# Kernel tuning notes

Measured on AMD Instinct MI355X. Metric: run time of the kernel, lower is better.

The kernel has to match this reference:

```python
import jax, jax.numpy as jnp
import numpy as np
from jax.ops import segment_sum

N = 100000
E = 1600000
D_IN = 64
D_H = 64
D_OUT = 16


def _gcn_norm(edge_index, n_nodes):
    # PyG GCNConv default: add self-loops, symmetric normalization.
    src, dst = edge_index[0], edge_index[1]
    loop = jnp.arange(n_nodes, dtype=edge_index.dtype)
    src = jnp.concatenate([src, loop])
    dst = jnp.concatenate([dst, loop])
    deg = segment_sum(jnp.ones(src.shape[0], dtype=jnp.float32), dst, num_segments=n_nodes)
    dinv = jnp.where(deg > 0, jax.lax.rsqrt(deg), 0.0)
    norm = dinv[src] * dinv[dst]  # [E + N]
    return src, dst, norm


def _gcn_layer(x, W, b, src, dst, norm, n_nodes):
    h = x @ W  # dense transform first (out_channels <= in_channels)
    msg = h[src] * norm[:, None]          # gather + scale  [E+N, out]
    agg = segment_sum(msg, dst, num_segments=n_nodes)  # scatter-add
    return agg + b


def setup_inputs() -> dict:
    key = jax.random.key(0)
    ks = jax.random.split(key, 10)
    x = jax.random.normal(ks[0], (N, D_IN), dtype=jnp.float32)
    edge_index = jax.random.randint(ks[1], (2, E), 0, N, dtype=jnp.int64)

    def glorot(k, fan_in, fan_out):
        lim = np.sqrt(6.0 / (fan_in + fan_out)).astype(np.float32)
        return jax.random.uniform(k, (fan_in, fan_out), jnp.float32, -lim, lim)

    return {
        "x": x,
        "edge_index": edge_index,
        "W1": glorot(ks[2], D_IN, D_H), "b1": jnp.zeros((D_H,), jnp.float32),
        "W2": glorot(ks[3], D_H, D_H), "b2": jnp.zeros((D_H,), jnp.float32),
        "W3": glorot(ks[4], D_H, D_H), "b3": jnp.zeros((D_H,), jnp.float32),
        "W4": glorot(ks[5], D_H, D_OUT), "b4": jnp.zeros((D_OUT,), jnp.float32),
    }


def reference(x, edge_index, W1, b1, W2, b2, W3, b3, W4, b4):
    n = x.shape[0]
    src, dst, norm = _gcn_norm(edge_index, n)
    h = jax.nn.relu(_gcn_layer(x, W1, b1, src, dst, norm, n))
    h = jax.nn.relu(_gcn_layer(h, W2, b2, src, dst, norm, n))
    h = jax.nn.relu(_gcn_layer(h, W3, b3, src, dst, norm, n))
    return _gcn_layer(h, W4, b4, src, dst, norm, n)
```

## Files before the change

kernel.cpp:

```cpp
#include <hip/hip_runtime.h>
#include <hip/hip_fp16.h>

#define NN 100000
#define NE 1600000
#define BK 256
#define BKSH 8
#define NBKT 391
#define SLOT 4608
#define SRCMASK 0x1FFFF

typedef _Float16 half2v __attribute__((ext_vector_type(2)));

__device__ inline float dot2acc(unsigned int a, unsigned int b, float c) {
#if __has_builtin(__builtin_amdgcn_fdot2)
    union { unsigned int u; half2v h; } ua, ub;
    ua.u = a; ub.u = b;
    return __builtin_amdgcn_fdot2(ua.h, ub.h, c, false);
#else
    float2 fa = __half22float2(*(const __half2*)&a);
    float2 fb = __half22float2(*(const __half2*)&b);
    return c + fa.x * fb.x + fa.y * fb.y;
#endif
}

__device__ inline int wave_incl_scan(int v, int lane) {
#pragma unroll
    for (int off = 1; off < 64; off <<= 1) {
        int t = __shfl_up(v, off, 64);
        if (lane >= off) v += t;
    }
    return v;
}


__global__ __launch_bounds__(512) void bscatter_kernel(const int* __restrict__ src,
                                                       const int* __restrict__ dst,
                                                       int* __restrict__ cnt,
                                                       int* __restrict__ bcur,
                                                       unsigned int* __restrict__ bedges,
                                                       int e) {
    __shared__ int h[512];
    __shared__ int gb[512];
    int tid = threadIdx.x;
    int tile = blockIdx.x * 4096;
    int cnt_tile = min(4096, e - tile);
    h[tid] = 0;
    __syncthreads();
    unsigned int pk[8]; int rk[8], bk[8];
#pragma unroll
    for (int j = 0; j < 8; j++) {
        int li = tid + j * 512;
        if (li < cnt_tile) {
            int s = src[tile + li];
            int d = dst[tile + li];
            bk[j] = d >> BKSH;
            pk[j] = ((unsigned)(d & (BK - 1)) << 17) | (unsigned)s;
            rk[j] = atomicAdd(&h[bk[j]], 1);
            atomicAdd(&cnt[d], 1);
        } else bk[j] = -1;
    }
    __syncthreads();
    {
        int c = h[tid];
        if (c > 0) gb[tid] = atomicAdd(&bcur[tid], c);
    }
    __syncthreads();
#pragma unroll
    for (int j = 0; j < 8; j++)
        if (bk[j] >= 0)
            bedges[(size_t)bk[j] * SLOT + gb[bk[j]] + rk[j]] = pk[j];
}

__global__ __launch_bounds__(512) void bfill_kernel(const unsigned int* __restrict__ bedges,
                                                    const int* __restrict__ bcur,
                                                    const int* __restrict__ cnt,
                                                    const float* __restrict__ x,
                                                    int* __restrict__ start,
                                                    float* __restrict__ dinv,
                                                    int* __restrict__ csr,
                                                    __half* __restrict__ g) {
    __shared__ int lcnt[BK];
    __shared__ int lstart[BK];
    __shared__ int lcur[BK];
    int q = blockIdx.x, tid = threadIdx.x;
    size_t ebase = (size_t)q * SLOT;
    int ec = bcur[q];
    int nbase = q * BK;
    if (tid < BK) {
        int nd = nbase + tid;
        lcnt[tid] = (nd < NN) ? cnt[nd] : 0;
    }
    unsigned int pk[9];
#pragma unroll
    for (int k = 0; k < 9; k++) {
        int i = tid + k * 512;
        pk[k] = (i < ec) ? __builtin_nontemporal_load(&bedges[ebase + i]) : 0xFFFFFFFFu;
    }
    __syncthreads();
    if (tid < 64) {
        int b0 = tid * 4;
        int c0 = lcnt[b0], c1 = lcnt[b0 + 1], c2 = lcnt[b0 + 2], c3 = lcnt[b0 + 3];
        int s4 = c0 + c1 + c2 + c3;
        int incl = wave_incl_scan(s4, tid);
        int base = incl - s4;
        lstart[b0] = base;               lcur[b0] = base;
        lstart[b0 + 1] = base + c0;      lcur[b0 + 1] = base + c0;
        lstart[b0 + 2] = base + c0 + c1; lcur[b0 + 2] = base + c0 + c1;
        lstart[b0 + 3] = base + c0 + c1 + c2; lcur[b0 + 3] = base + c0 + c1 + c2;
    }
    __syncthreads();
    if (tid < BK) {
        int nd = nbase + tid;
        if (nd < NN) {
            start[nd] = (int)ebase + lstart[tid];
            dinv[nd]  = rsqrtf((float)lcnt[tid] + 1.0f);
        }
    }
#pragma unroll
    for (int k = 0; k < 9; k++) {
        if (pk[k] != 0xFFFFFFFFu) {
            int r = atomicAdd(&lcur[pk[k] >> 17], 1);
            csr[ebase + r] = (int)(pk[k] & SRCMASK);
        }
    }
    int nh = NN - nbase; if (nh > BK) nh = BK;
    for (int i = tid; i < nh * 16; i += 512) {
        int r = i >> 4, c4 = (i & 15) << 2;
        float dvv = rsqrtf((float)lcnt[r] + 1.0f);
        size_t off = (size_t)(nbase + r) * 64 + c4;
        float4 v = *(const float4*)&x[off];
        union { __half2 h[2]; uint2 u; } pq;
        pq.h[0] = __floats2half2_rn(v.x * dvv, v.y * dvv);
        pq.h[1] = __floats2half2_rn(v.z * dvv, v.w * dvv);
        *(uint2*)&g[off] = pq.u;
    }
}

__global__ __launch_bounds__(512) void fused_layer_kernel(const __half* __restrict__ g,
                                                          const int* __restrict__ csr,
                                                          const int* __restrict__ start,
                                                          const int* __restrict__ cnt,
                                                          const float* __restrict__ dinv,
                                                          const float* __restrict__ Wg,
                                                          const float* __restrict__ bias,
                                                          __half* __restrict__ gout, int n) {
    __shared__ uint4 wpk[8][64];
    __shared__ __half zh[8][64];
    __shared__ float bs[64];
    int tid = threadIdx.x;
    {
        int p = tid >> 6, c = tid & 63;
        float w[8];
#pragma unroll
        for (int i = 0; i < 8; i++) w[i] = Wg[(8 * p + i) * 64 + c];
        union { __half2 h; unsigned int u; } u0, u1, u2, u3;
        u0.h = __floats2half2_rn(w[0], w[1]);
        u1.h = __floats2half2_rn(w[2], w[3]);
        u2.h = __floats2half2_rn(w[4], w[5]);
        u3.h = __floats2half2_rn(w[6], w[7]);
        wpk[p][c] = make_uint4(u0.u, u1.u, u2.u, u3.u);
    }
    if (tid < 64) bs[tid] = bias[tid];
    __syncthreads();

    int wv = tid >> 6, lane = tid & 63;
    int node = blockIdx.x * 8 + wv;
    float acc = 0.f;
    float dv = 0.f;
    if (node < n) {
        int st = __builtin_amdgcn_readfirstlane(start[node]);
        int cn = __builtin_amdgcn_readfirstlane(cnt[node]);
        dv = dinv[node];
        acc = __half2float(g[(size_t)node * 64 + lane]);
        int e = 0;
        for (; e + 7 < cn; e += 8) {
            int u[8]; float a[8];
#pragma unroll
            for (int j = 0; j < 8; j++) u[j] = __builtin_nontemporal_load(&csr[st + e + j]);
#pragma unroll
            for (int j = 0; j < 8; j++) a[j] = __half2float(g[(size_t)u[j] * 64 + lane]);
            acc += ((a[0] + a[1]) + (a[2] + a[3])) + ((a[4] + a[5]) + (a[6] + a[7]));
        }
        for (; e + 3 < cn; e += 4) {
            int u0 = __builtin_nontemporal_load(&csr[st + e + 0]);
            int u1 = __builtin_nontemporal_load(&csr[st + e + 1]);
            int u2 = __builtin_nontemporal_load(&csr[st + e + 2]);
            int u3 = __builtin_nontemporal_load(&csr[st + e + 3]);
            float a0 = __half2float(g[(size_t)u0 * 64 + lane]);
            float a1 = __half2float(g[(size_t)u1 * 64 + lane]);
            float a2 = __half2float(g[(size_t)u2 * 64 + lane]);
            float a3 = __half2float(g[(size_t)u3 * 64 + lane]);
            acc += (a0 + a1) + (a2 + a3);
        }
        for (; e < cn; e++) {
            int u = __builtin_nontemporal_load(&csr[st + e]);
            acc += __half2float(g[(size_t)u * 64 + lane]);
        }
    }
    zh[wv][lane] = __float2half_rn(acc);
    if (node < n) {
        float t = 0.f;
#pragma unroll
        for (int p = 0; p < 8; p++) {
            uint4 wq = wpk[p][lane];
            uint4 zq = *(const uint4*)&zh[wv][p * 8];
            t = dot2acc(zq.x, wq.x, t);
            t = dot2acc(zq.y, wq.y, t);
            t = dot2acc(zq.z, wq.z, t);
            t = dot2acc(zq.w, wq.w, t);
        }
        float o = dv * t + bs[lane];
        o = fmaxf(o, 0.f);
        gout[(size_t)node * 64 + lane] = __float2half_rn(dv * o);
    }
}

__global__ __launch_bounds__(512) void fused_last_kernel(const __half* __restrict__ g,
                                                         const int* __restrict__ csr,
                                                         const int* __restrict__ start,
                                                         const int* __restrict__ cnt,
                                                         const float* __restrict__ dinv,
                                                         const float* __restrict__ Wg,
                                                         const float* __restrict__ bias,
                                                         const float* __restrict__ W4,
                                                         __half* __restrict__ s4out, int n) {
    __shared__ uint4 wpk[8][64];
    __shared__ __half zh[8][64];
    __shared__ __half z2[8][64];
    __shared__ uint4 w4pk[8][16];
    __shared__ float bs[64];
    int tid = threadIdx.x;
    {
        int p = tid >> 6, c = tid & 63;
        float w[8];
#pragma unroll
        for (int i = 0; i < 8; i++) w[i] = Wg[(8 * p + i) * 64 + c];
        union { __half2 h; unsigned int u; } u0, u1, u2, u3;
        u0.h = __floats2half2_rn(w[0], w[1]);
        u1.h = __floats2half2_rn(w[2], w[3]);
        u2.h = __floats2half2_rn(w[4], w[5]);
        u3.h = __floats2half2_rn(w[6], w[7]);
        wpk[p][c] = make_uint4(u0.u, u1.u, u2.u, u3.u);
    }
    if (tid < 128) {
        int p = tid >> 4, j = tid & 15;
        float w[8];
#pragma unroll
        for (int i = 0; i < 8; i++) w[i] = W4[(8 * p + i) * 16 + j];
        union { __half2 h; unsigned int u; } u0, u1, u2, u3;
        u0.h = __floats2half2_rn(w[0], w[1]);
        u1.h = __floats2half2_rn(w[2], w[3]);
        u2.h = __floats2half2_rn(w[4], w[5]);
        u3.h = __floats2half2_rn(w[6], w[7]);
        w4pk[p][j] = make_uint4(u0.u, u1.u, u2.u, u3.u);
    }
    if (tid < 64) bs[tid] = bias[tid];
    __syncthreads();

    int wv = tid >> 6, lane = tid & 63;
    int node = blockIdx.x * 8 + wv;
    float acc = 0.f;
    float dv = 0.f;
    if (node < n) {
        int st = __builtin_amdgcn_readfirstlane(start[node]);
        int cn = __builtin_amdgcn_readfirstlane(cnt[node]);
        dv = dinv[node];
        acc = __half2float(g[(size_t)node * 64 + lane]);
        int e = 0;
        for (; e + 7 < cn; e += 8) {
            int u[8]; float a[8];
#pragma unroll
            for (int j = 0; j < 8; j++) u[j] = __builtin_nontemporal_load(&csr[st + e + j]);
#pragma unroll
            for (int j = 0; j < 8; j++) a[j] = __half2float(g[(size_t)u[j] * 64 + lane]);
            acc += ((a[0] + a[1]) + (a[2] + a[3])) + ((a[4] + a[5]) + (a[6] + a[7]));
        }
        for (; e + 3 < cn; e += 4) {
            int u0 = __builtin_nontemporal_load(&csr[st + e + 0]);
            int u1 = __builtin_nontemporal_load(&csr[st + e + 1]);
            int u2 = __builtin_nontemporal_load(&csr[st + e + 2]);
            int u3 = __builtin_nontemporal_load(&csr[st + e + 3]);
            float a0 = __half2float(g[(size_t)u0 * 64 + lane]);
            float a1 = __half2float(g[(size_t)u1 * 64 + lane]);
            float a2 = __half2float(g[(size_t)u2 * 64 + lane]);
            float a3 = __half2float(g[(size_t)u3 * 64 + lane]);
            acc += (a0 + a1) + (a2 + a3);
        }
        for (; e < cn; e++) {
            int u = __builtin_nontemporal_load(&csr[st + e]);
            acc += __half2float(g[(size_t)u * 64 + lane]);
        }
    }
    zh[wv][lane] = __float2half_rn(acc);
    if (node < n) {
        float t = 0.f;
#pragma unroll
        for (int p = 0; p < 8; p++) {
            uint4 wq = wpk[p][lane];
            uint4 zq = *(const uint4*)&zh[wv][p * 8];
            t = dot2acc(zq.x, wq.x, t);
            t = dot2acc(zq.y, wq.y, t);
            t = dot2acc(zq.z, wq.z, t);
            t = dot2acc(zq.w, wq.w, t);
        }
        float o = dv * t + bs[lane];
        o = fmaxf(o, 0.f);
        z2[wv][lane] = __float2half_rn(dv * o);
        int col = lane & 15, seg = lane >> 4;
        float t4 = 0.f;
#pragma unroll
        for (int pp = 0; pp < 2; pp++) {
            int p = seg * 2 + pp;
            uint4 wq = w4pk[p][col];
            uint4 zq = *(const uint4*)&z2[wv][p * 8];
            t4 = dot2acc(zq.x, wq.x, t4);
            t4 = dot2acc(zq.y, wq.y, t4);
            t4 = dot2acc(zq.z, wq.z, t4);
            t4 = dot2acc(zq.w, wq.w, t4);
        }
        t4 += __shfl_xor(t4, 16, 64);
        t4 += __shfl_xor(t4, 32, 64);
        if (lane < 16)
            s4out[(size_t)node * 16 + col] = __float2half_rn(t4);
    }
}

__global__ __launch_bounds__(256) void agg16_kernel(const __half* __restrict__ s,
                                                    const int* __restrict__ csr,
                                                    const int* __restrict__ start,
                                                    const int* __restrict__ cnt,
                                                    const float* __restrict__ dinv,
                                                    const float* __restrict__ bias,
                                                    float* __restrict__ out, int n) {
    constexpr int D = 16;
    int tid = threadIdx.x;
    int lane = tid & 63;
    int wave = tid >> 6;
    int col = lane % D;
    int grp = lane / D;
    int node = (blockIdx.x * 4 + wave) * 4 + grp;
    if (node >= n) return;
    int st = start[node];
    int cn = cnt[node];
    float acc = __half2float(s[(size_t)node * D + col]);
    int e = 0;
    for (; e + 7 < cn; e += 8) {
        int u[8]; float a[8];
#pragma unroll
        for (int j = 0; j < 8; j++) u[j] = __builtin_nontemporal_load(&csr[st + e + j]);
#pragma unroll
        for (int j = 0; j < 8; j++) a[j] = __half2float(s[(size_t)u[j] * D + col]);
        acc += ((a[0] + a[1]) + (a[2] + a[3])) + ((a[4] + a[5]) + (a[6] + a[7]));
    }
    for (; e + 3 < cn; e += 4) {
        int u0 = __builtin_nontemporal_load(&csr[st + e + 0]);
        int u1 = __builtin_nontemporal_load(&csr[st + e + 1]);
        int u2 = __builtin_nontemporal_load(&csr[st + e + 2]);
        int u3 = __builtin_nontemporal_load(&csr[st + e + 3]);
        float a0 = __half2float(s[(size_t)u0 * D + col]);
        float a1 = __half2float(s[(size_t)u1 * D + col]);
        float a2 = __half2float(s[(size_t)u2 * D + col]);
        float a3 = __half2float(s[(size_t)u3 * D + col]);
        acc += (a0 + a1) + (a2 + a3);
    }
    for (; e < cn; e++) {
        int u = __builtin_nontemporal_load(&csr[st + e]);
        acc += __half2float(s[(size_t)u * D + col]);
    }
    float o = dinv[node] * acc + bias[col];
    __builtin_nontemporal_store(o, out + (size_t)node * D + col);
}


extern "C" void kernel_launch(void* const* d_in, const int* in_sizes, int n_in,
                              void* d_out, int out_size, void* d_ws, size_t ws_size,
                              hipStream_t stream) {
    const float* x  = (const float*)d_in[0];
    const int* ei   = (const int*)d_in[1];
    const float* W1 = (const float*)d_in[2];
    const float* b1 = (const float*)d_in[3];
    const float* W2 = (const float*)d_in[4];
    const float* b2 = (const float*)d_in[5];
    const float* W3 = (const float*)d_in[6];
    const float* b3 = (const float*)d_in[7];
    const float* W4 = (const float*)d_in[8];
    const float* b4 = (const float*)d_in[9];
    const int* src = ei;
    const int* dst = ei + NE;

    char* w = (char*)d_ws;
    float* dinv  = (float*)w;          w += (size_t)NN * 4;
    int* cnt     = (int*)w;            w += (size_t)NN * 4;
    int* bcur    = (int*)w;            w += (size_t)512 * 4;
    int* start   = (int*)w;            w += (size_t)NN * 4;
    int* csr     = (int*)w;            w += (size_t)NBKT * SLOT * 4;
    __half* gA   = (__half*)w;         w += (size_t)NN * 64 * 2;
    __half* gB   = (__half*)w;         w += (size_t)NN * 64 * 2;
    __half* s4   = (__half*)w;         w += (size_t)NN * 16 * 2;
    unsigned int* bedges = (unsigned int*)w;  w += (size_t)NBKT * SLOT * 4;

    hipMemsetAsync(cnt, 0, (size_t)NN * 4 + 512 * 4, stream);
    bscatter_kernel<<<(NE + 4095) / 4096, 512, 0, stream>>>(src, dst, cnt, bcur, bedges, NE);
    bfill_kernel<<<NBKT, 512, 0, stream>>>(bedges, bcur, cnt, x, start, dinv, csr, gA);

    const int FB = (NN + 7) / 8;
    fused_layer_kernel<<<FB, 512, 0, stream>>>(gA, csr, start, cnt, dinv, W1, b1, gB, NN);
    fused_layer_kernel<<<FB, 512, 0, stream>>>(gB, csr, start, cnt, dinv, W2, b2, gA, NN);
    fused_last_kernel<<<FB, 512, 0, stream>>>(gA, csr, start, cnt, dinv, W3, b3, W4, s4, NN);

    const int AB16 = (NN + 15) / 16;
    agg16_kernel<<<AB16, 256, 0, stream>>>(s4, csr, start, cnt, dinv, b4, (float*)d_out, NN);
}
```

Baseline: 364.7 us.

## Count degrees in shared memory and gather two neighbors per wave with half2 loads

Degree counting moves out of the global-atomic scatter pass and into the per-bucket fill kernel, where it uses shared-memory atomics over the bucket's edges. That removes 1.6M global atomics and shrinks the memset to just the bucket cursors. The aggregation loops in the fused layer kernels now split each wave into two 32-lane halves, each loading half2 pairs from a different neighbor, then combine with a cross-half shuffle. This issues fewer, wider gather loads per edge, at the cost of a shuffle reduction and more register pressure from the 16-edge unroll.

```diff
diff --git a/kernel.cpp b/kernel.cpp
--- a/kernel.cpp
+++ b/kernel.cpp
@@ -35,7 +35,6 @@
 
 __global__ __launch_bounds__(512) void bscatter_kernel(const int* __restrict__ src,
                                                        const int* __restrict__ dst,
-                                                       int* __restrict__ cnt,
                                                        int* __restrict__ bcur,
                                                        unsigned int* __restrict__ bedges,
                                                        int e) {
@@ -56,7 +55,6 @@
             bk[j] = d >> BKSH;
             pk[j] = ((unsigned)(d & (BK - 1)) << 17) | (unsigned)s;
             rk[j] = atomicAdd(&h[bk[j]], 1);
-            atomicAdd(&cnt[d], 1);
         } else bk[j] = -1;
     }
     __syncthreads();
@@ -73,9 +71,9 @@
 
 __global__ __launch_bounds__(512) void bfill_kernel(const unsigned int* __restrict__ bedges,
                                                     const int* __restrict__ bcur,
-                                                    const int* __restrict__ cnt,
                                                     const float* __restrict__ x,
                                                     int* __restrict__ start,
+                                                    int* __restrict__ cnt,
                                                     float* __restrict__ dinv,
                                                     int* __restrict__ csr,
                                                     __half* __restrict__ g) {
@@ -86,16 +84,17 @@
     size_t ebase = (size_t)q * SLOT;
     int ec = bcur[q];
     int nbase = q * BK;
-    if (tid < BK) {
-        int nd = nbase + tid;
-        lcnt[tid] = (nd < NN) ? cnt[nd] : 0;
-    }
+    if (tid < BK) lcnt[tid] = 0;
+    __syncthreads();
     unsigned int pk[9];
 #pragma unroll
     for (int k = 0; k < 9; k++) {
         int i = tid + k * 512;
         pk[k] = (i < ec) ? __builtin_nontemporal_load(&bedges[ebase + i]) : 0xFFFFFFFFu;
     }
+#pragma unroll
+    for (int k = 0; k < 9; k++)
+        if (pk[k] != 0xFFFFFFFFu) atomicAdd(&lcnt[pk[k] >> 17], 1);
     __syncthreads();
     if (tid < 64) {
         int b0 = tid * 4;
@@ -113,6 +112,7 @@
         int nd = nbase + tid;
         if (nd < NN) {
             start[nd] = (int)ebase + lstart[tid];
+            cnt[nd]   = lcnt[tid];
             dinv[nd]  = rsqrtf((float)lcnt[tid] + 1.0f);
         }
     }
@@ -164,40 +164,66 @@
     __syncthreads();
 
     int wv = tid >> 6, lane = tid & 63;
+    int hv = lane >> 5;
+    int c2 = lane & 31;
     int node = blockIdx.x * 8 + wv;
-    float acc = 0.f;
-    float dv = 0.f;
+    float ax = 0.f, ay = 0.f, dv = 0.f;
     if (node < n) {
         int st = __builtin_amdgcn_readfirstlane(start[node]);
         int cn = __builtin_amdgcn_readfirstlane(cnt[node]);
         dv = dinv[node];
-        acc = __half2float(g[(size_t)node * 64 + lane]);
+        {
+            unsigned int sv = *(const unsigned int*)(g + (size_t)node * 64 + 2 * c2);
+            float2 sf = __half22float2(*(const __half2*)&sv);
+            if (hv == 0) { ax = sf.x; ay = sf.y; }
+        }
         int e = 0;
+        for (; e + 15 < cn; e += 16) {
+            int u[16];
+#pragma unroll
+            for (int j = 0; j < 16; j++) u[j] = __builtin_nontemporal_load(&csr[st + e + j]);
+            float2 f[8];
+#pragma unroll
+            for (int j = 0; j < 8; j++) {
+                int us = hv ? u[2 * j + 1] : u[2 * j];
+                unsigned int v = *(const unsigned int*)(g + (size_t)us * 64 + 2 * c2);
+                f[j] = __half22float2(*(const __half2*)&v);
+            }
+            ax += ((f[0].x + f[1].x) + (f[2].x + f[3].x)) + ((f[4].x + f[5].x) + (f[6].x + f[7].x));
+            ay += ((f[0].y + f[1].y) + (f[2].y + f[3].y)) + ((f[4].y + f[5].y) + (f[6].y + f[7].y));
+        }
         for (; e + 7 < cn; e += 8) {
-            int u[8]; float a[8];
+            int u[8];
 #pragma unroll
             for (int j = 0; j < 8; j++) u[j] = __builtin_nontemporal_load(&csr[st + e + j]);
-#pragma unroll
-            for (int j = 0; j < 8; j++) a[j] = __half2float(g[(size_t)u[j] * 64 + lane]);
-            acc += ((a[0] + a[1]) + (a[2] + a[3])) + ((a[4] + a[5]) + (a[6] + a[7]));
-        }
-        for (; e + 3 < cn; e += 4) {
-            int u0 = __builtin_nontemporal_load(&csr[st + e + 0]);
+            float2 f[4];
+#pragma unroll
+            for (int j = 0; j < 4; j++) {
+                int us = hv ? u[2 * j + 1] : u[2 * j];
+                unsigned int v = *(const unsigned int*)(g + (size_t)us * 64 + 2 * c2);
+                f[j] = __half22float2(*(const __half2*)&v);
+            }
+            ax += (f[0].x + f[1].x) + (f[2].x + f[3].x);
+            ay += (f[0].y + f[1].y) + (f[2].y + f[3].y);
+        }
+        for (; e + 1 < cn; e += 2) {
+            int u0 = __builtin_nontemporal_load(&csr[st + e]);
             int u1 = __builtin_nontemporal_load(&csr[st + e + 1]);
-            int u2 = __builtin_nontemporal_load(&csr[st + e + 2]);
-            int u3 = __builtin_nontemporal_load(&csr[st + e + 3]);
-            float a0 = __half2float(g[(size_t)u0 * 64 + lane]);
-            float a1 = __half2float(g[(size_t)u1 * 64 + lane]);
-            float a2 = __half2float(g[(size_t)u2 * 64 + lane]);
-            float a3 = __half2float(g[(size_t)u3 * 64 + lane]);
-            acc += (a0 + a1) + (a2 + a3);
-        }
-        for (; e < cn; e++) {
-            int u = __builtin_nontemporal_load(&csr[st + e]);
-            acc += __half2float(g[(size_t)u * 64 + lane]);
-        }
-    }
-    zh[wv][lane] = __float2half_rn(acc);
+            int us = hv ? u1 : u0;
+            unsigned int v = *(const unsigned int*)(g + (size_t)us * 64 + 2 * c2);
+            float2 f = __half22float2(*(const __half2*)&v);
+            ax += f.x; ay += f.y;
+        }
+        if (e < cn) {
+            int u0 = __builtin_nontemporal_load(&csr[st + e]);
+            unsigned int v = *(const unsigned int*)(g + (size_t)u0 * 64 + 2 * c2);
+            float2 f = __half22float2(*(const __half2*)&v);
+            if (hv == 0) { ax += f.x; ay += f.y; }
+        }
+        ax += __shfl_xor(ax, 32, 64);
+        ay += __shfl_xor(ay, 32, 64);
+    }
+    *(__half2*)&zh[wv][2 * c2] = __floats2half2_rn(ax, ay);
     if (node < n) {
         float t = 0.f;
 #pragma unroll
@@ -258,40 +284,66 @@
     __syncthreads();
 
     int wv = tid >> 6, lane = tid & 63;
+    int hv = lane >> 5;
+    int c2 = lane & 31;
     int node = blockIdx.x * 8 + wv;
-    float acc = 0.f;
-    float dv = 0.f;
+    float ax = 0.f, ay = 0.f, dv = 0.f;
     if (node < n) {
         int st = __builtin_amdgcn_readfirstlane(start[node]);
         int cn = __builtin_amdgcn_readfirstlane(cnt[node]);
         dv = dinv[node];
-        acc = __half2float(g[(size_t)node * 64 + lane]);
+        {
+            unsigned int sv = *(const unsigned int*)(g + (size_t)node * 64 + 2 * c2);
+            float2 sf = __half22float2(*(const __half2*)&sv);
+            if (hv == 0) { ax = sf.x; ay = sf.y; }
+        }
         int e = 0;
+        for (; e + 15 < cn; e += 16) {
+            int u[16];
+#pragma unroll
+            for (int j = 0; j < 16; j++) u[j] = __builtin_nontemporal_load(&csr[st + e + j]);
+            float2 f[8];
+#pragma unroll
+            for (int j = 0; j < 8; j++) {
+                int us = hv ? u[2 * j + 1] : u[2 * j];
+                unsigned int v = *(const unsigned int*)(g + (size_t)us * 64 + 2 * c2);
+                f[j] = __half22float2(*(const __half2*)&v);
+            }
+            ax += ((f[0].x + f[1].x) + (f[2].x + f[3].x)) + ((f[4].x + f[5].x) + (f[6].x + f[7].x));
+            ay += ((f[0].y + f[1].y) + (f[2].y + f[3].y)) + ((f[4].y + f[5].y) + (f[6].y + f[7].y));
+        }
         for (; e + 7 < cn; e += 8) {
-            int u[8]; float a[8];
+            int u[8];
 #pragma unroll
             for (int j = 0; j < 8; j++) u[j] = __builtin_nontemporal_load(&csr[st + e + j]);
-#pragma unroll
-            for (int j = 0; j < 8; j++) a[j] = __half2float(g[(size_t)u[j] * 64 + lane]);
-            acc += ((a[0] + a[1]) + (a[2] + a[3])) + ((a[4] + a[5]) + (a[6] + a[7]));
-        }
-        for (; e + 3 < cn; e += 4) {
-            int u0 = __builtin_nontemporal_load(&csr[st + e + 0]);
+            float2 f[4];
+#pragma unroll
+            for (int j = 0; j < 4; j++) {
+                int us = hv ? u[2 * j + 1] : u[2 * j];
+                unsigned int v = *(const unsigned int*)(g + (size_t)us * 64 + 2 * c2);
+                f[j] = __half22float2(*(const __half2*)&v);
+            }
+            ax += (f[0].x + f[1].x) + (f[2].x + f[3].x);
+            ay += (f[0].y + f[1].y) + (f[2].y + f[3].y);
+        }
+        for (; e + 1 < cn; e += 2) {
+            int u0 = __builtin_nontemporal_load(&csr[st + e]);
             int u1 = __builtin_nontemporal_load(&csr[st + e + 1]);
-            int u2 = __builtin_nontemporal_load(&csr[st + e + 2]);
-            int u3 = __builtin_nontemporal_load(&csr[st + e + 3]);
-            float a0 = __half2float(g[(size_t)u0 * 64 + lane]);
-            float a1 = __half2float(g[(size_t)u1 * 64 + lane]);
-            float a2 = __half2float(g[(size_t)u2 * 64 + lane]);
-            float a3 = __half2float(g[(size_t)u3 * 64 + lane]);
-            acc += (a0 + a1) + (a2 + a3);
-        }
-        for (; e < cn; e++) {
-            int u = __builtin_nontemporal_load(&csr[st + e]);
-            acc += __half2float(g[(size_t)u * 64 + lane]);
-        }
-    }
-    zh[wv][lane] = __float2half_rn(acc);
+            int us = hv ? u1 : u0;
+            unsigned int v = *(const unsigned int*)(g + (size_t)us * 64 + 2 * c2);
+            float2 f = __half22float2(*(const __half2*)&v);
+            ax += f.x; ay += f.y;
+        }
+        if (e < cn) {
+            int u0 = __builtin_nontemporal_load(&csr[st + e]);
+            unsigned int v = *(const unsigned int*)(g + (size_t)u0 * 64 + 2 * c2);
+            float2 f = __half22float2(*(const __half2*)&v);
+            if (hv == 0) { ax += f.x; ay += f.y; }
+        }
+        ax += __shfl_xor(ax, 32, 64);
+        ay += __shfl_xor(ay, 32, 64);
+    }
+    *(__half2*)&zh[wv][2 * c2] = __floats2half2_rn(ax, ay);
     if (node < n) {
         float t = 0.f;
 #pragma unroll
@@ -391,17 +443,17 @@
     char* w = (char*)d_ws;
     float* dinv  = (float*)w;          w += (size_t)NN * 4;
     int* cnt     = (int*)w;            w += (size_t)NN * 4;
+    int* start   = (int*)w;            w += (size_t)NN * 4;
     int* bcur    = (int*)w;            w += (size_t)512 * 4;
-    int* start   = (int*)w;            w += (size_t)NN * 4;
     int* csr     = (int*)w;            w += (size_t)NBKT * SLOT * 4;
     __half* gA   = (__half*)w;         w += (size_t)NN * 64 * 2;
     __half* gB   = (__half*)w;         w += (size_t)NN * 64 * 2;
     __half* s4   = (__half*)w;         w += (size_t)NN * 16 * 2;
     unsigned int* bedges = (unsigned int*)w;  w += (size_t)NBKT * SLOT * 4;
 
-    hipMemsetAsync(cnt, 0, (size_t)NN * 4 + 512 * 4, stream);
-    bscatter_kernel<<<(NE + 4095) / 4096, 512, 0, stream>>>(src, dst, cnt, bcur, bedges, NE);
-    bfill_kernel<<<NBKT, 512, 0, stream>>>(bedges, bcur, cnt, x, start, dinv, csr, gA);
+    hipMemsetAsync(bcur, 0, 512 * sizeof(int), stream);
+    bscatter_kernel<<<(NE + 4095) / 4096, 512, 0, stream>>>(src, dst, bcur, bedges, NE);
+    bfill_kernel<<<NBKT, 512, 0, stream>>>(bedges, bcur, x, start, cnt, dinv, csr, gA);
 
     const int FB = (NN + 7) / 8;
     fused_layer_kernel<<<FB, 512, 0, stream>>>(gA, csr, start, cnt, dinv, W1, b1, gB, NN);
```

After: 305.0 us (median of 2 runs). 16.4% less time.
